# Kernel tuning notes

Hardware: AMD Instinct MI355X
Metric: run time of the kernel (lower is better)

The kernel has to match this reference:

```python
import jax, jax.numpy as jnp
import numpy as np

T, B, C, H = 2048, 8, 512, 8
D = C // H  # head dim = 64


def setup_inputs() -> dict:
    key0 = jax.random.key(0)
    ks = jax.random.split(key0, 12)
    std = 0.02
    inp = {
        "query": jax.random.normal(ks[0], (T, B, C), dtype=jnp.float32),
        "key": jax.random.normal(ks[1], (T, B, C), dtype=jnp.float32),
        "value": jax.random.normal(ks[2], (T, B, C), dtype=jnp.float32),
        "Wq": jax.random.normal(ks[3], (C, C), dtype=jnp.float32) * std,
        "bq": jnp.zeros((C,), dtype=jnp.float32),
        "Wk": jax.random.normal(ks[4], (C, C), dtype=jnp.float32) * std,
        "bk": jnp.zeros((C,), dtype=jnp.float32),
        "Wv": jax.random.normal(ks[5], (C, C), dtype=jnp.float32) * std,
        "bv": jnp.zeros((C,), dtype=jnp.float32),
        "Wo": jax.random.normal(ks[6], (C, C), dtype=jnp.float32) * std,
        "bo": jnp.zeros((C,), dtype=jnp.float32),
    }
    return inp


def reference(query, key, value, Wq, bq, Wk, bk, Wv, bv, Wo, bo):
    # batch_first=False: incoming [T, B, C] -> [B, T, C]
    q_in = jnp.transpose(query, (1, 0, 2))
    k_in = jnp.transpose(key, (1, 0, 2))
    v_in = jnp.transpose(value, (1, 0, 2))

    # nn.Linear: x @ W.T + b, then split heads -> [B, H, T, D]
    def proj(x, W, b):
        y = x @ W.T + b
        return y.reshape(x.shape[0], x.shape[1], H, D).transpose(0, 2, 1, 3)

    q = proj(q_in, Wq, bq)
    k = proj(k_in, Wk, bk)
    v = proj(v_in, Wv, bv)

    # scaled_query_key_softmax: q / sqrt(D), attn_mask=None, dropout p=0 is identity
    scale = 1.0 / jnp.sqrt(jnp.asarray(D, dtype=q.dtype))
    att = jnp.einsum("bhqd,bhkd->bhqk", q * scale, k)
    att = jax.nn.softmax(att, axis=-1)
    y = jnp.einsum("bhqk,bhkd->bhqd", att, v)  # [B, H, T, D]

    # merge heads -> [B, T, C], output projection, back to [T, B, C]
    y = y.transpose(0, 2, 1, 3).reshape(q_in.shape[0], q_in.shape[1], C)
    out = y @ Wo.T + bo
    return jnp.transpose(out, (1, 0, 2))
```

## Files before the change

kernel.cpp:

```cpp
#include <hip/hip_runtime.h>

#define TT 2048
#define BB 8
#define CC 512
#define HH 8
#define DD 64
#define MM (TT*BB)
#define LDP 72
#define QSCALE (0.125f * 1.44269950408889634f)

#define OFF_WQ 0u
#define OFF_WK (512u<<10)
#define OFF_WV (1024u<<10)
#define OFF_WO (1536u<<10)
#define OFF_Q  (2u<<20)
#define OFF_K  (18u<<20)
#define OFF_VT (34u<<20)
#define OFF_V  (50u<<20)
#define OFF_Y  OFF_V

typedef __attribute__((ext_vector_type(8)))  unsigned short us8;
typedef __attribute__((ext_vector_type(4)))  unsigned short us4;
typedef __attribute__((ext_vector_type(4)))  float f4;
typedef __bf16 bf8v __attribute__((ext_vector_type(8)));

__device__ __forceinline__ unsigned short f2bf(float f) {
  unsigned u = __float_as_uint(f);
  u += 0x7fffu + ((u >> 16) & 1u);
  return (unsigned short)(u >> 16);
}

__device__ __forceinline__ f4 MFMA(us8 a, us8 b, f4 c) {
  return __builtin_amdgcn_mfma_f32_16x16x32_bf16(
      __builtin_bit_cast(bf8v, a), __builtin_bit_cast(bf8v, b), c, 0, 0, 0);
}

__global__ __launch_bounds__(256) void prep_w(const float* wq, const float* wk,
                                              const float* wv, const float* wo,
                                              unsigned short* dst) {
  int i = blockIdx.x * 256 + threadIdx.x;
  const float* srcs[4] = {wq, wk, wv, wo};
#pragma unroll
  for (int m = 0; m < 4; m++) {
    f4 v = ((const f4*)srcs[m])[i];
    us4 o;
    o[0] = f2bf(v[0]); o[1] = f2bf(v[1]); o[2] = f2bf(v[2]); o[3] = f2bf(v[3]);
    ((us4*)(dst + m * 262144))[i] = o;
  }
}

template <bool XF32>
__device__ __forceinline__ void gemm_core(const void* Xv, const unsigned short* W,
                                          int m0, int n0, f4 acc[4][4],
                                          unsigned short* XsL, unsigned short* WsL) {
  const int tid = threadIdx.x;
  const int w = tid >> 6, lane = tid & 63, g = lane >> 4, l16 = lane & 15;
  const int wr = w >> 1, wc = w & 1;
#pragma unroll
  for (int m = 0; m < 4; m++)
#pragma unroll
    for (int n = 0; n < 4; n++) acc[m][n] = (f4){0.f, 0.f, 0.f, 0.f};

  for (int kk = 0; kk < CC; kk += 64) {
    __syncthreads();
#pragma unroll
    for (int i = 0; i < 4; i++) {
      int c = tid + 256 * i;
      int r = c >> 3, k8 = c & 7;
      if (XF32) {
        const float* src = (const float*)Xv + (size_t)(m0 + r) * CC + kk + k8 * 8;
        f4 v0 = ((const f4*)src)[0];
        f4 v1 = ((const f4*)src)[1];
        us8 o;
        o[0] = f2bf(v0[0]); o[1] = f2bf(v0[1]); o[2] = f2bf(v0[2]); o[3] = f2bf(v0[3]);
        o[4] = f2bf(v1[0]); o[5] = f2bf(v1[1]); o[6] = f2bf(v1[2]); o[7] = f2bf(v1[3]);
        *(us8*)(&XsL[r * LDP + k8 * 8]) = o;
      } else {
        const unsigned short* src = (const unsigned short*)Xv + (size_t)(m0 + r) * CC + kk + k8 * 8;
        *(us8*)(&XsL[r * LDP + k8 * 8]) = *(const us8*)src;
      }
    }
#pragma unroll
    for (int i = 0; i < 4; i++) {
      int c = tid + 256 * i;
      int r = c >> 3, k8 = c & 7;
      const unsigned short* src = W + (size_t)(n0 + r) * CC + kk + k8 * 8;
      *(us8*)(&WsL[r * LDP + k8 * 8]) = *(const us8*)src;
    }
    __syncthreads();
#pragma unroll
    for (int ks = 0; ks < 2; ks++) {
      us8 a[4], b[4];
#pragma unroll
      for (int m = 0; m < 4; m++)
        a[m] = *(const us8*)(&XsL[(wr * 64 + m * 16 + l16) * LDP + ks * 32 + g * 8]);
#pragma unroll
      for (int n = 0; n < 4; n++)
        b[n] = *(const us8*)(&WsL[(wc * 64 + n * 16 + l16) * LDP + ks * 32 + g * 8]);
#pragma unroll
      for (int m = 0; m < 4; m++)
#pragma unroll
        for (int n = 0; n < 4; n++)
          acc[m][n] = MFMA(a[m], b[n], acc[m][n]);
    }
  }
}

__global__ __launch_bounds__(256) void gemm_qkv(const float* xq, const float* xk, const float* xv,
                                                const float* bq, const float* bk, const float* bv,
                                                char* ws) {
  __shared__ unsigned short XsL[128 * LDP];
  __shared__ unsigned short WsL[128 * LDP];
  const int z = blockIdx.z;
  const float* X    = (z == 0) ? xq : (z == 1) ? xk : xv;
  const float* bias = (z == 0) ? bq : (z == 1) ? bk : bv;
  const unsigned short* W = (const unsigned short*)(ws + (size_t)z * 524288u);
  unsigned short* out = (unsigned short*)(ws + ((z == 0) ? OFF_Q : (z == 1) ? OFF_K : OFF_V));
  const float osc = (z == 0) ? QSCALE : 1.0f;

  const int m0 = blockIdx.x * 128, n0 = blockIdx.y * 128;
  f4 acc[4][4];
  gemm_core<true>(X, W, m0, n0, acc, XsL, WsL);

  const int tid = threadIdx.x, w = tid >> 6, lane = tid & 63, g = lane >> 4, l16 = lane & 15;
  const int wr = w >> 1, wc = w & 1;
#pragma unroll
  for (int n = 0; n < 4; n++) {
    int col = n0 + wc * 64 + n * 16 + l16;
    float bvv = bias[col];
    int h = col >> 6, d = col & 63;
#pragma unroll
    for (int m = 0; m < 4; m++) {
      int rbase = m0 + wr * 64 + m * 16 + 4 * g;
#pragma unroll
      for (int r = 0; r < 4; r++) {
        int row = rbase + r;
        int t = row >> 3, b = row & 7;
        float val = (acc[m][n][r] + bvv) * osc;
        out[(size_t)((b * HH + h) * TT + t) * DD + d] = f2bf(val);
      }
    }
  }
}

__global__ __launch_bounds__(256) void transpose_v(char* ws) {
  __shared__ unsigned short Ts[64 * LDP];
  const unsigned short* V = (const unsigned short*)(ws + OFF_V);
  unsigned short* Vt = (unsigned short*)(ws + OFF_VT);
  const int bh = blockIdx.y, t0 = blockIdx.x * 64;
  const int tid = threadIdx.x;
#pragma unroll
  for (int i = 0; i < 2; i++) {
    int c = tid + 256 * i;
    int r = c >> 3, k8 = c & 7;
    *(us8*)(&Ts[r * LDP + k8 * 8]) =
        *(const us8*)(V + (size_t)(bh * TT + t0 + r) * DD + k8 * 8);
  }
  __syncthreads();
#pragma unroll
  for (int i = 0; i < 2; i++) {
    int c = tid + 256 * i;
    int d = c >> 3, t8 = c & 7;
    us8 o;
#pragma unroll
    for (int j = 0; j < 8; j++) o[j] = Ts[(t8 * 8 + j) * LDP + d];
    *(us8*)(Vt + (size_t)(bh * DD + d) * TT + t0 + t8 * 8) = o;
  }
}

__global__ __launch_bounds__(256) void attn(char* ws) {
  __shared__ unsigned short Ks[64 * 64];
  __shared__ unsigned short Vs[64 * 64];
  __shared__ unsigned short Ps[4][16 * LDP];
  const unsigned short* Q  = (const unsigned short*)(ws + OFF_Q);
  const unsigned short* K  = (const unsigned short*)(ws + OFF_K);
  const unsigned short* Vt = (const unsigned short*)(ws + OFF_VT);
  unsigned short* Y = (unsigned short*)(ws + OFF_Y);

  const int bh = blockIdx.y, t0 = blockIdx.x * 64;
  const int tid = threadIdx.x, w = tid >> 6, lane = tid & 63, g = lane >> 4, l16 = lane & 15;

  const int qrow = t0 + w * 16 + l16;
  const unsigned short* qp = Q + (size_t)(bh * TT + qrow) * DD;
  us8 aq[2];
  aq[0] = *(const us8*)(qp + g * 8);
  aq[1] = *(const us8*)(qp + 32 + g * 8);

  f4 accy[4];
#pragma unroll
  for (int i = 0; i < 4; i++) accy[i] = (f4){0.f, 0.f, 0.f, 0.f};
  float rowsum[4] = {0.f, 0.f, 0.f, 0.f};

  const unsigned short* Kbh = K + (size_t)bh * TT * DD;
  const unsigned short* Vbh = Vt + (size_t)bh * DD * TT;

  for (int kt = 0; kt < TT; kt += 64) {
    __syncthreads();
#pragma unroll
    for (int i = 0; i < 2; i++) {
      int c = tid + 256 * i;
      int r = c >> 3, ch = c & 7;
      us8 v = *(const us8*)(Kbh + (size_t)(kt + r) * DD + ch * 8);
      int chs = ch ^ (r & 7);
      *(us8*)((char*)Ks + r * 128 + chs * 16) = v;
    }
#pragma unroll
    for (int i = 0; i < 2; i++) {
      int c = tid + 256 * i;
      int r = c >> 3, ch = c & 7;
      us8 v = *(const us8*)(Vbh + (size_t)r * TT + kt + ch * 8);
      int chs = ch ^ (r & 7);
      *(us8*)((char*)Vs + r * 128 + chs * 16) = v;
    }
    __syncthreads();

    f4 s[4];
#pragma unroll
    for (int nf = 0; nf < 4; nf++) {
      s[nf] = (f4){0.f, 0.f, 0.f, 0.f};
#pragma unroll
      for (int ks = 0; ks < 2; ks++) {
        int krow = nf * 16 + l16;
        us8 kb = *(const us8*)((char*)Ks + krow * 128 + (((ks * 4 + g) ^ (krow & 7)) * 16));
        s[nf] = MFMA(aq[ks], kb, s[nf]);
      }
    }

#pragma unroll
    for (int nf = 0; nf < 4; nf++) {
#pragma unroll
      for (int r = 0; r < 4; r++) {
        float p = exp2f(s[nf][r]);
        rowsum[r] += p;
        Ps[w][(4 * g + r) * LDP + l16 + 16 * nf] = f2bf(p);
      }
    }
    asm volatile("" ::: "memory");

    us8 ap[2];
    ap[0] = *(const us8*)(&Ps[w][l16 * LDP + g * 8]);
    ap[1] = *(const us8*)(&Ps[w][l16 * LDP + 32 + g * 8]);
#pragma unroll
    for (int nd = 0; nd < 4; nd++) {
#pragma unroll
      for (int ks = 0; ks < 2; ks++) {
        int drow = nd * 16 + l16;
        us8 vb = *(const us8*)((char*)Vs + drow * 128 + (((ks * 4 + g) ^ (drow & 7)) * 16));
        accy[nd] = MFMA(ap[ks], vb, accy[nd]);
      }
    }
  }

#pragma unroll
  for (int r = 0; r < 4; r++) {
    float v = rowsum[r];
    v += __shfl_xor(v, 1); v += __shfl_xor(v, 2);
    v += __shfl_xor(v, 4); v += __shfl_xor(v, 8);
    rowsum[r] = 1.0f / v;
  }

  const int b = bh >> 3, h = bh & 7;
#pragma unroll
  for (int nd = 0; nd < 4; nd++) {
    int d = l16 + 16 * nd;
#pragma unroll
    for (int r = 0; r < 4; r++) {
      int trow = t0 + w * 16 + 4 * g + r;
      Y[(size_t)(b * TT + trow) * CC + h * DD + d] = f2bf(accy[nd][r] * rowsum[r]);
    }
  }
}

__global__ __launch_bounds__(256) void gemm_oproj(char* ws, const float* bo, float* out) {
  __shared__ unsigned short XsL[128 * LDP];
  __shared__ unsigned short WsL[128 * LDP];
  const unsigned short* X = (const unsigned short*)(ws + OFF_Y);
  const unsigned short* W = (const unsigned short*)(ws + OFF_WO);
  const int m0 = blockIdx.x * 128, n0 = blockIdx.y * 128;
  f4 acc[4][4];
  gemm_core<false>(X, W, m0, n0, acc, XsL, WsL);

  const int tid = threadIdx.x, w = tid >> 6, lane = tid & 63, g = lane >> 4, l16 = lane & 15;
  const int wr = w >> 1, wc = w & 1;
#pragma unroll
  for (int n = 0; n < 4; n++) {
    int col = n0 + wc * 64 + n * 16 + l16;
    float bvv = bo[col];
#pragma unroll
    for (int m = 0; m < 4; m++) {
      int rbase = m0 + wr * 64 + m * 16 + 4 * g;
#pragma unroll
      for (int r = 0; r < 4; r++) {
        int row = rbase + r;
        int b = row >> 11, t = row & 2047;
        out[(size_t)(t * BB + b) * CC + col] = acc[m][n][r] + bvv;
      }
    }
  }
}

extern "C" void kernel_launch(void* const* d_in, const int* in_sizes, int n_in,
                              void* d_out, int out_size, void* d_ws, size_t ws_size,
                              hipStream_t stream) {
  const float* query = (const float*)d_in[0];
  const float* key_  = (const float*)d_in[1];
  const float* value = (const float*)d_in[2];
  const float* Wq = (const float*)d_in[3];
  const float* bq = (const float*)d_in[4];
  const float* Wk = (const float*)d_in[5];
  const float* bk = (const float*)d_in[6];
  const float* Wv = (const float*)d_in[7];
  const float* bv = (const float*)d_in[8];
  const float* Wo = (const float*)d_in[9];
  const float* bo = (const float*)d_in[10];
  char* ws = (char*)d_ws;

  prep_w<<<dim3(256), dim3(256), 0, stream>>>(Wq, Wk, Wv, Wo, (unsigned short*)ws);
  gemm_qkv<<<dim3(128, 4, 3), dim3(256), 0, stream>>>(query, key_, value, bq, bk, bv, ws);
  transpose_v<<<dim3(32, 64), dim3(256), 0, stream>>>(ws);
  attn<<<dim3(32, 64), dim3(256), 0, stream>>>(ws);
  gemm_oproj<<<dim3(128, 4), dim3(256), 0, stream>>>(ws, bo, (float*)d_out);
}
```

Baseline: 360.9 us.

## Restructure attention to 32x32 MFMA with register-resident P and larger query tiles

The attention kernel switches from 16x16x32 to 32x32x16 bf16 MFMA. It computes S transposed (K as the A operand) so the exponentiated probabilities can be packed with v_cvt_pk_bf16 and exchanged across half-waves with shuffles, with no LDS round-trip for P. Blocks grow to 512 threads covering 256 query rows, so each K/V tile staged in LDS is reused by four times as many queries. The cost is more register pressure from the 16-wide accumulators, fewer blocks in the grid, and cross-lane shuffles.

```diff
diff --git a/kernel.cpp b/kernel.cpp
--- a/kernel.cpp
+++ b/kernel.cpp
@@ -22,6 +22,8 @@
 typedef __attribute__((ext_vector_type(8)))  unsigned short us8;
 typedef __attribute__((ext_vector_type(4)))  unsigned short us4;
 typedef __attribute__((ext_vector_type(4)))  float f4;
+typedef __attribute__((ext_vector_type(16))) float f16v;
+typedef __attribute__((ext_vector_type(4)))  unsigned int u4;
 typedef __bf16 bf8v __attribute__((ext_vector_type(8)));
 
 __device__ __forceinline__ unsigned short f2bf(float f) {
@@ -33,6 +35,17 @@
 __device__ __forceinline__ f4 MFMA(us8 a, us8 b, f4 c) {
   return __builtin_amdgcn_mfma_f32_16x16x32_bf16(
       __builtin_bit_cast(bf8v, a), __builtin_bit_cast(bf8v, b), c, 0, 0, 0);
+}
+
+__device__ __forceinline__ f16v MFMA32(us8 a, us8 b, f16v c) {
+  return __builtin_amdgcn_mfma_f32_32x32x16_bf16(
+      __builtin_bit_cast(bf8v, a), __builtin_bit_cast(bf8v, b), c, 0, 0, 0);
+}
+
+__device__ __forceinline__ unsigned cvt_pk_bf16(float lo, float hi) {
+  unsigned r;
+  asm("v_cvt_pk_bf16_f32 %0, %1, %2" : "=v"(r) : "v"(lo), "v"(hi));
+  return r;
 }
 
 __global__ __launch_bounds__(256) void prep_w(const float* wq, const float* wk,
@@ -168,105 +181,107 @@
   }
 }
 
-__global__ __launch_bounds__(256) void attn(char* ws) {
+__global__ __launch_bounds__(512) void attn(char* ws) {
   __shared__ unsigned short Ks[64 * 64];
   __shared__ unsigned short Vs[64 * 64];
-  __shared__ unsigned short Ps[4][16 * LDP];
+  __shared__ float Rs[8 * 32];
   const unsigned short* Q  = (const unsigned short*)(ws + OFF_Q);
   const unsigned short* K  = (const unsigned short*)(ws + OFF_K);
   const unsigned short* Vt = (const unsigned short*)(ws + OFF_VT);
   unsigned short* Y = (unsigned short*)(ws + OFF_Y);
 
-  const int bh = blockIdx.y, t0 = blockIdx.x * 64;
-  const int tid = threadIdx.x, w = tid >> 6, lane = tid & 63, g = lane >> 4, l16 = lane & 15;
-
-  const int qrow = t0 + w * 16 + l16;
-  const unsigned short* qp = Q + (size_t)(bh * TT + qrow) * DD;
-  us8 aq[2];
-  aq[0] = *(const us8*)(qp + g * 8);
-  aq[1] = *(const us8*)(qp + 32 + g * 8);
-
-  f4 accy[4];
-#pragma unroll
-  for (int i = 0; i < 4; i++) accy[i] = (f4){0.f, 0.f, 0.f, 0.f};
-  float rowsum[4] = {0.f, 0.f, 0.f, 0.f};
+  const int bh = blockIdx.y, t0 = blockIdx.x * 256;
+  const int tid = threadIdx.x, w = tid >> 6, lane = tid & 63;
+  const int l31 = lane & 31, h = lane >> 5;
+  const int swz = l31 & 7;
 
   const unsigned short* Kbh = K + (size_t)bh * TT * DD;
   const unsigned short* Vbh = Vt + (size_t)bh * DD * TT;
 
+  const int qrow = t0 + w * 32 + l31;
+  const unsigned short* qp = Q + ((size_t)bh * TT + qrow) * DD + h * 8;
+  us8 qf[4];
+#pragma unroll
+  for (int ks = 0; ks < 4; ks++) qf[ks] = *(const us8*)(qp + ks * 16);
+
+  f16v accy[2];
+#pragma unroll
+  for (int i = 0; i < 16; i++) { accy[0][i] = 0.f; accy[1][i] = 0.f; }
+  float rsum = 0.f;
+
+  const int sr = tid >> 3, sch = tid & 7, schs = sch ^ (sr & 7);
+  const unsigned short* Kg = Kbh + (size_t)sr * DD + sch * 8;
+  const unsigned short* Vg = Vbh + (size_t)sr * TT + sch * 8;
+  char* kdst = (char*)Ks + sr * 128 + schs * 16;
+  char* vdst = (char*)Vs + sr * 128 + schs * 16;
+
   for (int kt = 0; kt < TT; kt += 64) {
     __syncthreads();
-#pragma unroll
-    for (int i = 0; i < 2; i++) {
-      int c = tid + 256 * i;
-      int r = c >> 3, ch = c & 7;
-      us8 v = *(const us8*)(Kbh + (size_t)(kt + r) * DD + ch * 8);
-      int chs = ch ^ (r & 7);
-      *(us8*)((char*)Ks + r * 128 + chs * 16) = v;
-    }
-#pragma unroll
-    for (int i = 0; i < 2; i++) {
-      int c = tid + 256 * i;
-      int r = c >> 3, ch = c & 7;
-      us8 v = *(const us8*)(Vbh + (size_t)r * TT + kt + ch * 8);
-      int chs = ch ^ (r & 7);
-      *(us8*)((char*)Vs + r * 128 + chs * 16) = v;
-    }
+    *(us8*)kdst = *(const us8*)(Kg + (size_t)kt * DD);
+    *(us8*)vdst = *(const us8*)(Vg + kt);
     __syncthreads();
 
-    f4 s[4];
-#pragma unroll
-    for (int nf = 0; nf < 4; nf++) {
-      s[nf] = (f4){0.f, 0.f, 0.f, 0.f};
-#pragma unroll
-      for (int ks = 0; ks < 2; ks++) {
-        int krow = nf * 16 + l16;
-        us8 kb = *(const us8*)((char*)Ks + krow * 128 + (((ks * 4 + g) ^ (krow & 7)) * 16));
-        s[nf] = MFMA(aq[ks], kb, s[nf]);
-      }
-    }
-
-#pragma unroll
-    for (int nf = 0; nf < 4; nf++) {
-#pragma unroll
-      for (int r = 0; r < 4; r++) {
-        float p = exp2f(s[nf][r]);
-        rowsum[r] += p;
-        Ps[w][(4 * g + r) * LDP + l16 + 16 * nf] = f2bf(p);
-      }
-    }
-    asm volatile("" ::: "memory");
-
-    us8 ap[2];
-    ap[0] = *(const us8*)(&Ps[w][l16 * LDP + g * 8]);
-    ap[1] = *(const us8*)(&Ps[w][l16 * LDP + 32 + g * 8]);
-#pragma unroll
-    for (int nd = 0; nd < 4; nd++) {
-#pragma unroll
-      for (int ks = 0; ks < 2; ks++) {
-        int drow = nd * 16 + l16;
-        us8 vb = *(const us8*)((char*)Vs + drow * 128 + (((ks * 4 + g) ^ (drow & 7)) * 16));
-        accy[nd] = MFMA(ap[ks], vb, accy[nd]);
-      }
-    }
-  }
-
-#pragma unroll
-  for (int r = 0; r < 4; r++) {
-    float v = rowsum[r];
-    v += __shfl_xor(v, 1); v += __shfl_xor(v, 2);
-    v += __shfl_xor(v, 4); v += __shfl_xor(v, 8);
-    rowsum[r] = 1.0f / v;
-  }
-
-  const int b = bh >> 3, h = bh & 7;
-#pragma unroll
-  for (int nd = 0; nd < 4; nd++) {
-    int d = l16 + 16 * nd;
-#pragma unroll
-    for (int r = 0; r < 4; r++) {
-      int trow = t0 + w * 16 + 4 * g + r;
-      Y[(size_t)(b * TT + trow) * CC + h * DD + d] = f2bf(accy[nd][r] * rowsum[r]);
+#pragma unroll
+    for (int f = 0; f < 2; f++) {
+      f16v s;
+#pragma unroll
+      for (int i = 0; i < 16; i++) s[i] = 0.f;
+#pragma unroll
+      for (int ks = 0; ks < 4; ks++) {
+        us8 kf = *(const us8*)((char*)Ks + (f * 32 + l31) * 128 + (((ks * 2 + h) ^ swz) * 16));
+        s = MFMA32(kf, qf[ks], s);
+      }
+      float p[16];
+#pragma unroll
+      for (int r = 0; r < 16; r++) {
+        p[r] = __builtin_amdgcn_exp2f(s[r]);
+        rsum += p[r];
+      }
+      unsigned dc0[4], dc1[4];
+#pragma unroll
+      for (int q2 = 0; q2 < 4; q2++) {
+        dc0[q2] = cvt_pk_bf16(p[4 * q2 + 0], p[4 * q2 + 1]);
+        dc1[q2] = cvt_pk_bf16(p[4 * q2 + 2], p[4 * q2 + 3]);
+      }
+#pragma unroll
+      for (int kss = 0; kss < 2; kss++) {
+        int ks = f * 2 + kss;
+        unsigned z0 = h ? dc0[2 * kss + 1] : dc0[2 * kss];
+        unsigned y0 = h ? dc0[2 * kss]     : dc0[2 * kss + 1];
+        unsigned z1 = h ? dc1[2 * kss + 1] : dc1[2 * kss];
+        unsigned y1 = h ? dc1[2 * kss]     : dc1[2 * kss + 1];
+        unsigned s0 = __shfl_xor(y0, 32);
+        unsigned s1 = __shfl_xor(y1, 32);
+        unsigned w0 = h ? s0 : z0;
+        unsigned w1 = h ? s1 : z1;
+        unsigned w2 = h ? z0 : s0;
+        unsigned w3 = h ? z1 : s1;
+        u4 av = (u4){w0, w1, w2, w3};
+        us8 af = __builtin_bit_cast(us8, av);
+#pragma unroll
+        for (int nd = 0; nd < 2; nd++) {
+          us8 vb = *(const us8*)((char*)Vs + (nd * 32 + l31) * 128 + (((ks * 2 + h) ^ swz) * 16));
+          accy[nd] = MFMA32(af, vb, accy[nd]);
+        }
+      }
+    }
+  }
+
+  rsum += __shfl_xor(rsum, 32);
+  float inv = 1.0f / rsum;
+  if (h == 0) Rs[w * 32 + l31] = inv;
+  __syncthreads();
+
+  const int b = bh >> 3, hh = bh & 7;
+#pragma unroll
+  for (int nd = 0; nd < 2; nd++) {
+    int d = nd * 32 + l31;
+#pragma unroll
+    for (int r = 0; r < 16; r++) {
+      int q = 8 * (r >> 2) + 4 * h + (r & 3);
+      int trow = t0 + w * 32 + q;
+      float v = accy[nd][r] * Rs[w * 32 + q];
+      Y[(size_t)(b * TT + trow) * CC + hh * DD + d] = f2bf(v);
     }
   }
 }
@@ -318,6 +333,6 @@
   prep_w<<<dim3(256), dim3(256), 0, stream>>>(Wq, Wk, Wv, Wo, (unsigned short*)ws);
   gemm_qkv<<<dim3(128, 4, 3), dim3(256), 0, stream>>>(query, key_, value, bq, bk, bv, ws);
   transpose_v<<<dim3(32, 64), dim3(256), 0, stream>>>(ws);
-  attn<<<dim3(32, 64), dim3(256), 0, stream>>>(ws);
+  attn<<<dim3(8, 64), dim3(512), 0, stream>>>(ws);
   gemm_oproj<<<dim3(128, 4), dim3(256), 0, stream>>>(ws, bo, (float*)d_out);
 }
```

After: 294.6 us. -18.4%, faster.
